# Kernel tuning notes

Hardware: AMD Instinct MI355X
Metric: run time of the kernel (lower is better)

Reference implementation:

```python
import jax, jax.numpy as jnp
import numpy as np

H, B, GH = 4096, 8192, 1024
TEMP = 1.0


def setup_inputs() -> dict:
    key = jax.random.key(0)
    ks = jax.random.split(key, 8)
    return {
        "hidden_states": jax.random.normal(ks[0], (B, H), jnp.float32),
        "attention_mask": jax.random.randint(ks[1], (B,), 0, 2) > 0,
        # similarity_proj: init N(0, 0.02); value_proj: nonzero randoms so kernel math is exercised
        "W_sim": jax.random.normal(ks[2], (H, H), jnp.float32) * 0.02,
        "W_val": jax.random.normal(ks[3], (H, H), jnp.float32) * 0.02,
        # gate_net: Linear(2H, GH) -> GELU -> Linear(GH, H) -> Sigmoid
        "W_g1": jax.random.normal(ks[4], (GH, 2 * H), jnp.float32) * 0.01,
        "b_g1": jnp.zeros((GH,), jnp.float32),
        "W_g2": jax.random.normal(ks[5], (H, GH), jnp.float32) * 0.01,
        "b_g2": jnp.full((H,), -3.0, jnp.float32),
    }


def reference(hidden_states, attention_mask, W_sim, W_val, W_g1, b_g1, W_g2, b_g2):
    b = hidden_states.shape[0]
    # similarity projection + L2 normalize (F.normalize, eps=1e-12)
    proj = hidden_states @ W_sim.T                                  # [B, H]
    norm = jnp.maximum(jnp.linalg.norm(proj, axis=-1, keepdims=True), 1e-12)
    normed = proj / norm
    sim = (normed @ normed.T) / TEMP                                # [B, B]
    # mask self (eye) and invalid samples (columns)
    eye = jnp.eye(b, dtype=bool)
    sim = jnp.where(eye | ~attention_mask[None, :], -jnp.inf, sim)
    weights = jax.nn.softmax(sim, axis=-1)
    weights = jnp.nan_to_num(weights, nan=0.0)
    values = hidden_states @ W_val.T                                # [B, H]
    cross = weights @ values                                        # [B, H]
    # question-aware gate: sigmoid(MLP(cat(h, cross)))
    gate_in = jnp.concatenate([hidden_states, cross], axis=-1)      # [B, 2H]
    h1 = jax.nn.gelu(gate_in @ W_g1.T + b_g1, approximate=False)    # exact GELU (torch default)
    gate = jax.nn.sigmoid(h1 @ W_g2.T + b_g2)                       # [B, H]
    return hidden_states + gate * cross
```

## Files before the change

### kernel.cpp

```cpp
#include <hip/hip_runtime.h>


#define HDIM 4096
#define BATCH 8192
#define GHDIM 1024

typedef unsigned short u16;
typedef short bf16x8 __attribute__((ext_vector_type(8)));
typedef float f32x4 __attribute__((ext_vector_type(4)));

__device__ __forceinline__ u16 f2bf(float f) {
  union { float f; unsigned u; } v; v.f = f;
  unsigned r = v.u + 0x7FFFu + ((v.u >> 16) & 1u);
  return (u16)(r >> 16);
}
__device__ __forceinline__ float bf2f(u16 u) {
  union { unsigned u; float f; } v; v.u = ((unsigned)u) << 16;
  return v.f;
}

__global__ void cast_f32_bf16(const float* __restrict__ src, u16* __restrict__ dst, int n4) {
  int i = blockIdx.x * 256 + threadIdx.x;
  if (i < n4) {
    float4 f = ((const float4*)src)[i];
    ushort4 o;
    o.x = f2bf(f.x); o.y = f2bf(f.y); o.z = f2bf(f.z); o.w = f2bf(f.w);
    ((ushort4*)dst)[i] = o;
  }
}

__global__ void detect_mask(const unsigned char* __restrict__ m, int nbytes, int* __restrict__ flag) {
  __shared__ int cnt[256];
  int c = 0;
  for (int i = threadIdx.x; i < nbytes; i += 256)
    if ((i & 3) && m[i]) c++;
  cnt[threadIdx.x] = c;
  __syncthreads();
  for (int s = 128; s > 0; s >>= 1) {
    if ((int)threadIdx.x < s) cnt[threadIdx.x] += cnt[threadIdx.x + s];
    __syncthreads();
  }
  if (threadIdx.x == 0) *flag = cnt[0];
}

__global__ void compact_mask(const void* __restrict__ raw, const int* __restrict__ flag,
                             int* __restrict__ idxc, int* __restrict__ kinfo) {
  const int t = threadIdx.x;
  const bool isbool = (*flag > 0);
  __shared__ int cnt[256];
  __shared__ int total;
  const int base0 = t * 32;
  int c = 0;
  for (int i = 0; i < 32; i++) {
    int gi = base0 + i;
    int v = isbool ? ((const unsigned char*)raw)[gi] : ((const int*)raw)[gi];
    if (v) c++;
  }
  cnt[t] = c;
  __syncthreads();
  if (t == 0) {
    int acc = 0;
    for (int i = 0; i < 256; i++) { int x = cnt[i]; cnt[i] = acc; acc += x; }
    total = acc;
    kinfo[0] = acc;
    kinfo[1] = (acc + 255) & ~255;
  }
  __syncthreads();
  int w = cnt[t];
  for (int i = 0; i < 32; i++) {
    int gi = base0 + i;
    int v = isbool ? ((const unsigned char*)raw)[gi] : ((const int*)raw)[gi];
    if (v) idxc[w++] = gi;
  }
  for (int i = total + t; i < BATCH; i += 256) idxc[i] = -1;
}

__global__ void gather_rows(const u16* __restrict__ src, u16* __restrict__ dst,
                            const int* __restrict__ idxc, const int* __restrict__ kinfo) {
  int c = blockIdx.x;
  int kc = kinfo[0], kp = kinfo[1];
  if (c >= kp) return;
  uint4* d = (uint4*)(dst + (size_t)c * HDIM);
  if (c < kc) {
    const uint4* s = (const uint4*)(src + (size_t)idxc[c] * HDIM);
    d[threadIdx.x] = s[threadIdx.x];
    d[threadIdx.x + 256] = s[threadIdx.x + 256];
  } else {
    uint4 z = {0, 0, 0, 0};
    d[threadIdx.x] = z;
    d[threadIdx.x + 256] = z;
  }
}

__global__ void normalize_rows(u16* __restrict__ p) {
  int row = blockIdx.x;
  uint4* r = (uint4*)(p + (size_t)row * HDIM);
  uint4 d[2];
  float s = 0.f;
#pragma unroll
  for (int i = 0; i < 2; i++) {
    d[i] = r[i * 256 + threadIdx.x];
    const u16* u = (const u16*)&d[i];
#pragma unroll
    for (int j = 0; j < 8; j++) { float f = bf2f(u[j]); s += f * f; }
  }
  __shared__ float red[256];
  red[threadIdx.x] = s;
  __syncthreads();
  for (int st = 128; st > 0; st >>= 1) {
    if ((int)threadIdx.x < st) red[threadIdx.x] += red[threadIdx.x + st];
    __syncthreads();
  }
  float scale = 1.0f / fmaxf(sqrtf(red[0]), 1e-12f);
#pragma unroll
  for (int i = 0; i < 2; i++) {
    u16* u = (u16*)&d[i];
#pragma unroll
    for (int j = 0; j < 8; j++) u[j] = f2bf(bf2f(u[j]) * scale);
    r[i * 256 + threadIdx.x] = d[i];
  }
}

__global__ void softmax_rows_dyn(u16* __restrict__ sim, const int* __restrict__ kinfo) {
  const int kp = kinfo[1];
  const int row = blockIdx.x;
  uint4* r = (uint4*)(sim + (size_t)row * BATCH);
  float v[32];
  int active[4];
  float mx = -3.0e38f;
#pragma unroll
  for (int ch = 0; ch < 4; ch++) {
    int base = ch * 2048 + threadIdx.x * 8;
    active[ch] = (base < kp);
    if (active[ch]) {
      uint4 d = r[ch * 256 + threadIdx.x];
      const u16* u = (const u16*)&d;
#pragma unroll
      for (int j = 0; j < 8; j++) {
        float f = bf2f(u[j]);
        v[ch * 8 + j] = f;
        mx = fmaxf(mx, f);
      }
    }
  }
  __shared__ float red[256];
  red[threadIdx.x] = mx;
  __syncthreads();
  for (int st = 128; st > 0; st >>= 1) {
    if ((int)threadIdx.x < st) red[threadIdx.x] = fmaxf(red[threadIdx.x], red[threadIdx.x + st]);
    __syncthreads();
  }
  mx = red[0];
  __syncthreads();
  float s = 0.f;
#pragma unroll
  for (int ch = 0; ch < 4; ch++) {
    if (active[ch]) {
#pragma unroll
      for (int j = 0; j < 8; j++) {
        float e = (v[ch * 8 + j] < -1.0e30f) ? 0.f : __expf(v[ch * 8 + j] - mx);
        v[ch * 8 + j] = e;
        s += e;
      }
    }
  }
  red[threadIdx.x] = s;
  __syncthreads();
  for (int st = 128; st > 0; st >>= 1) {
    if ((int)threadIdx.x < st) red[threadIdx.x] += red[threadIdx.x + st];
    __syncthreads();
  }
  float inv = (red[0] > 0.f) ? 1.0f / red[0] : 0.f;
#pragma unroll
  for (int ch = 0; ch < 4; ch++) {
    if (active[ch]) {
      uint4 d;
      u16* u = (u16*)&d;
#pragma unroll
      for (int j = 0; j < 8; j++) u[j] = f2bf(v[ch * 8 + j] * inv);
      r[ch * 256 + threadIdx.x] = d;
    }
  }
}

enum { EPI_BF16 = 0, EPI_SIM = 1, EPI_F32 = 2, EPI_GELU = 3, EPI_FINAL = 4 };

__device__ __forceinline__ void async_load16(const u16* g, u16* l) {
  __builtin_amdgcn_global_load_lds(
      (const __attribute__((address_space(1))) void*)g,
      (__attribute__((address_space(3))) void*)l, 16, 0, 0);
}

template <int EPI>
__global__ __launch_bounds__(512, 2) void gemm256(
    const u16* __restrict__ A, int lda,
    const u16* __restrict__ B, int ldb,
    void* __restrict__ C, int ldc,
    int M, int N, int K,
    const int* __restrict__ kinfo, int dynN, int dynK,
    const int* __restrict__ idxc,
    const float* __restrict__ aux,
    const u16* __restrict__ aux2,
    const float* __restrict__ bias) {
  const int nwg = (int)(gridDim.x * gridDim.y);
  const int orig = (int)(blockIdx.y * gridDim.x + blockIdx.x);
  int wgid;
  {
    int q = nwg >> 3, r = nwg & 7, x = orig & 7, lo = orig >> 3;
    wgid = (x < r ? x * (q + 1) : r * (q + 1) + (x - r) * q) + lo;
  }
  const int bx = wgid % (int)gridDim.x;
  const int by = wgid / (int)gridDim.x;
  const int rowBase = by * 256;
  const int colBase = bx * 256;
  if (dynN && colBase >= kinfo[1]) return;
  const int Keff = dynK ? kinfo[1] : K;
  const int NT = Keff >> 5;

  __shared__ __align__(16) u16 sm[4 * 16384];

  const int tid = threadIdx.x;
  const int lane = tid & 63, wave = tid >> 6;
  const int wm = wave >> 2, wn = wave & 3;
  const int fr = lane & 15, kq = lane >> 4;

  int aOff[8], bOff[4];
#pragma unroll
  for (int mi = 0; mi < 8; mi++) {
    int lin = ((wm * 8 + mi) << 10) + (fr << 6) + (kq << 4);
    aOff[mi] = lin ^ (((fr >> 3) & 1) << 5);
  }
#pragma unroll
  for (int ni = 0; ni < 4; ni++) {
    int lin = ((wn * 4 + ni) << 10) + (fr << 6) + (kq << 4);
    bOff[ni] = (lin ^ (((fr >> 3) & 1) << 5)) + 16384;
  }

  const int i0row = wave * 16 + (lane >> 2);
  const int scol = ((lane & 3) << 3) ^ (((lane >> 5) & 1) << 4);

  auto stageA = [&](int tt) {
    const int sb = (tt & 3) * 16384;
    const int kt = tt << 5;
#pragma unroll
    for (int i = 0; i < 2; i++)
      async_load16(A + (size_t)(rowBase + i * 128 + i0row) * lda + kt + scol,
                   sm + sb + i * 4096 + tid * 8);
  };
  auto stageB = [&](int tt) {
    const int sb = (tt & 3) * 16384 + 8192;
    const int kt = tt << 5;
#pragma unroll
    for (int i = 0; i < 2; i++)
      async_load16(B + (size_t)(colBase + i * 128 + i0row) * ldb + kt + scol,
                   sm + sb + i * 4096 + tid * 8);
  };

  f32x4 zero = {0.f, 0.f, 0.f, 0.f};
  f32x4 acc[8][4];
#pragma unroll
  for (int mi = 0; mi < 8; mi++)
#pragma unroll
    for (int ni = 0; ni < 4; ni++) acc[mi][ni] = zero;

  if (NT > 0) { stageA(0); stageB(0); }
  if (NT > 1) { stageA(1); stageB(1); }
  if (NT > 2) { stageA(2); stageB(2); }
  if (NT >= 3)      asm volatile("s_waitcnt vmcnt(8)" ::: "memory");
  else if (NT == 2) asm volatile("s_waitcnt vmcnt(4)" ::: "memory");
  else              asm volatile("s_waitcnt vmcnt(0)" ::: "memory");
  __builtin_amdgcn_sched_barrier(0);
  __builtin_amdgcn_s_barrier();

  for (int t = 0; t < NT; ++t) {
    const char* slot = (const char*)sm + (size_t)(t & 3) * 32768;
    const int pt = t + 3;
    const bool pf = pt < NT;

    bf16x8 af[4], bf[4];
#pragma unroll
    for (int mi = 0; mi < 4; mi++) af[mi] = *(const bf16x8*)(slot + aOff[mi]);
#pragma unroll
    for (int ni = 0; ni < 4; ni++) bf[ni] = *(const bf16x8*)(slot + bOff[ni]);
    if (pf) stageA(pt);
    __builtin_amdgcn_s_barrier();
    __builtin_amdgcn_s_setprio(1);
#pragma unroll
    for (int mi = 0; mi < 4; mi++)
#pragma unroll
      for (int ni = 0; ni < 4; ni++)
        acc[mi][ni] = __builtin_amdgcn_mfma_f32_16x16x32_bf16(af[mi], bf[ni], acc[mi][ni], 0, 0, 0);
    __builtin_amdgcn_s_setprio(0);
    __builtin_amdgcn_s_barrier();

#pragma unroll
    for (int mi = 0; mi < 4; mi++) af[mi] = *(const bf16x8*)(slot + aOff[mi + 4]);
    if (pf) stageB(pt);
    __builtin_amdgcn_s_barrier();
    __builtin_amdgcn_s_setprio(1);
#pragma unroll
    for (int mi = 0; mi < 4; mi++)
#pragma unroll
      for (int ni = 0; ni < 4; ni++)
        acc[mi + 4][ni] = __builtin_amdgcn_mfma_f32_16x16x32_bf16(af[mi], bf[ni], acc[mi + 4][ni], 0, 0, 0);
    __builtin_amdgcn_s_setprio(0);
    if (pf)                asm volatile("s_waitcnt vmcnt(8)" ::: "memory");
    else if (t + 2 < NT)   asm volatile("s_waitcnt vmcnt(4)" ::: "memory");
    else if (t + 1 < NT)   asm volatile("s_waitcnt vmcnt(0)" ::: "memory");
    __builtin_amdgcn_sched_barrier(0);
    __builtin_amdgcn_s_barrier();
  }

  const int quad = lane >> 4, lcol = lane & 15;
#pragma unroll
  for (int mi = 0; mi < 8; mi++) {
#pragma unroll
    for (int ni = 0; ni < 4; ni++) {
#pragma unroll
      for (int r = 0; r < 4; r++) {
        int grow = rowBase + wm * 128 + mi * 16 + quad * 4 + r;
        int gcol = colBase + wn * 64 + ni * 16 + lcol;
        float v = acc[mi][ni][r];
        size_t idx = (size_t)grow * ldc + gcol;
        if constexpr (EPI == EPI_BF16) {
          ((u16*)C)[idx] = f2bf(v);
        } else if constexpr (EPI == EPI_SIM) {
          bool dead = (gcol >= kinfo[0]) || (idxc[gcol] == grow);
          ((u16*)C)[idx] = dead ? (u16)0xFF80 : f2bf(v);
        } else if constexpr (EPI == EPI_F32) {
          ((float*)C)[idx] = v;
        } else if constexpr (EPI == EPI_GELU) {
          float x = v + aux[idx] + bias[gcol];
          float g = 0.5f * x * (1.0f + erff(x * 0.70710678118654752f));
          ((u16*)C)[idx] = f2bf(g);
        } else {
          float x = v + bias[gcol];
          float g = 1.0f / (1.0f + __expf(-x));
          ((float*)C)[idx] = aux[idx] + g * bf2f(aux2[idx]);
        }
      }
    }
  }
}

template <int EPI>
__global__ __launch_bounds__(256) void gemm_bt(
    const u16* __restrict__ A, int lda,
    const u16* __restrict__ B, int ldb,
    void* __restrict__ C, int ldc,
    int M, int N, int K,
    const int* __restrict__ kinfo, int dynN, int dynK,
    const int* __restrict__ idxc,
    const float* __restrict__ aux,
    const u16* __restrict__ aux2,
    const float* __restrict__ bias) {
  const int rowBase = blockIdx.y * 128;
  const int colBase = blockIdx.x * 128;
  if (dynN && colBase >= kinfo[1]) return;
  const int Keff = dynK ? kinfo[1] : K;

  __shared__ __align__(16) u16 lA[128 * 64];
  __shared__ __align__(16) u16 lB[128 * 64];
  const int tid = threadIdx.x;
  const int lane = tid & 63;
  const int wave = tid >> 6;
  const int waveRow = (wave >> 1) * 64;
  const int waveCol = (wave & 1) * 64;

  const u16* Ab = A + (size_t)rowBase * lda;
  const u16* Bb = B + (size_t)colBase * ldb;

  f32x4 zero = {0.f, 0.f, 0.f, 0.f};
  f32x4 acc[4][4];
#pragma unroll
  for (int mi = 0; mi < 4; mi++)
#pragma unroll
    for (int ni = 0; ni < 4; ni++) acc[mi][ni] = zero;

  for (int kt = 0; kt < Keff; kt += 64) {
#pragma unroll
    for (int i = 0; i < 4; i++) {
      int c = i * 256 + tid;
      int row = c >> 3, k8 = c & 7;
      int gk8 = k8 ^ (row & 7);
      async_load16(Ab + (size_t)row * lda + kt + gk8 * 8, &lA[c * 8]);
    }
#pragma unroll
    for (int i = 0; i < 4; i++) {
      int c = i * 256 + tid;
      int row = c >> 3, k8 = c & 7;
      int gk8 = k8 ^ (row & 7);
      async_load16(Bb + (size_t)row * ldb + kt + gk8 * 8, &lB[c * 8]);
    }
    __syncthreads();
#pragma unroll
    for (int ks = 0; ks < 2; ks++) {
      const int kq = ks * 4 + (lane >> 4);
      bf16x8 af[4], bfr[4];
#pragma unroll
      for (int mi = 0; mi < 4; mi++) {
        int row = waveRow + mi * 16 + (lane & 15);
        af[mi] = *(const bf16x8*)&lA[row * 64 + ((kq ^ (row & 7)) * 8)];
      }
#pragma unroll
      for (int ni = 0; ni < 4; ni++) {
        int row = waveCol + ni * 16 + (lane & 15);
        bfr[ni] = *(const bf16x8*)&lB[row * 64 + ((kq ^ (row & 7)) * 8)];
      }
#pragma unroll
      for (int mi = 0; mi < 4; mi++)
#pragma unroll
        for (int ni = 0; ni < 4; ni++)
          acc[mi][ni] = __builtin_amdgcn_mfma_f32_16x16x32_bf16(af[mi], bfr[ni], acc[mi][ni], 0, 0, 0);
    }
    __syncthreads();
  }

  const int quad = lane >> 4, lcol = lane & 15;
#pragma unroll
  for (int mi = 0; mi < 4; mi++) {
#pragma unroll
    for (int ni = 0; ni < 4; ni++) {
#pragma unroll
      for (int r = 0; r < 4; r++) {
        int grow = rowBase + waveRow + mi * 16 + quad * 4 + r;
        int gcol = colBase + waveCol + ni * 16 + lcol;
        float v = acc[mi][ni][r];
        size_t idx = (size_t)grow * ldc + gcol;
        if constexpr (EPI == EPI_BF16) {
          ((u16*)C)[idx] = f2bf(v);
        } else if constexpr (EPI == EPI_SIM) {
          bool dead = (gcol >= kinfo[0]) || (idxc[gcol] == grow);
          ((u16*)C)[idx] = dead ? (u16)0xFF80 : f2bf(v);
        } else if constexpr (EPI == EPI_F32) {
          ((float*)C)[idx] = v;
        } else if constexpr (EPI == EPI_GELU) {
          float x = v + aux[idx] + bias[gcol];
          float g = 0.5f * x * (1.0f + erff(x * 0.70710678118654752f));
          ((u16*)C)[idx] = f2bf(g);
        } else {
          float x = v + bias[gcol];
          float g = 1.0f / (1.0f + __expf(-x));
          ((float*)C)[idx] = aux[idx] + g * bf2f(aux2[idx]);
        }
      }
    }
  }
}

extern "C" void kernel_launch(void* const* d_in, const int* in_sizes, int n_in,
                              void* d_out, int out_size, void* d_ws, size_t ws_size,
                              hipStream_t stream) {
  const float* hs   = (const float*)d_in[0];
  const void*  mraw = d_in[1];
  const float* Wsim = (const float*)d_in[2];
  const float* Wval = (const float*)d_in[3];
  const float* Wg1  = (const float*)d_in[4];
  const float* bg1  = (const float*)d_in[5];
  const float* Wg2  = (const float*)d_in[6];
  const float* bg2  = (const float*)d_in[7];
  float* out = (float*)d_out;

  char* ws = (char*)d_ws;
  size_t off = 0;
  auto alloc = [&](size_t bytes) {
    char* p = ws + off;
    off += (bytes + 255) & ~(size_t)255;
    return p;
  };
  u16* hidden_bf = (u16*)alloc((size_t)BATCH * HDIM * 2);
  u16* wbuf      = (u16*)alloc((size_t)HDIM * HDIM * 2);
  u16* r1        = (u16*)alloc((size_t)BATCH * HDIM * 2);
  u16* r2        = (u16*)alloc((size_t)BATCH * HDIM * 2);
  int* idxc      = (int*)alloc((size_t)BATCH * 4);
  int* kinfo     = (int*)alloc(256);
  int* flag      = (int*)alloc(256);
  if (off > ws_size) return;

  u16*   simw  = (u16*)d_out;
  float* h1acc = (float*)d_out;
  (void)in_sizes; (void)n_in; (void)out_size;

  dim3 blk(256);
  dim3 blk5(512);

  detect_mask<<<1, 256, 0, stream>>>((const unsigned char*)mraw, BATCH, flag);
  compact_mask<<<1, 256, 0, stream>>>(mraw, flag, idxc, kinfo);

  cast_f32_bf16<<<(BATCH * HDIM / 4) / 256, 256, 0, stream>>>(hs, hidden_bf, BATCH * HDIM / 4);

  cast_f32_bf16<<<(HDIM * HDIM / 4) / 256, 256, 0, stream>>>(Wsim, wbuf, HDIM * HDIM / 4);
  gemm256<EPI_BF16><<<dim3(HDIM / 256, BATCH / 256), blk5, 0, stream>>>(
      hidden_bf, HDIM, wbuf, HDIM, r1, HDIM, BATCH, HDIM, HDIM,
      nullptr, 0, 0, nullptr, nullptr, nullptr, nullptr);
  normalize_rows<<<BATCH, 256, 0, stream>>>(r1);

  gather_rows<<<BATCH, 256, 0, stream>>>(r1, r2, idxc, kinfo);

  gemm256<EPI_SIM><<<dim3(BATCH / 256, BATCH / 256), blk5, 0, stream>>>(
      r1, HDIM, r2, HDIM, simw, BATCH, BATCH, BATCH, HDIM,
      kinfo, 1, 0, idxc, nullptr, nullptr, nullptr);
  softmax_rows_dyn<<<BATCH, 256, 0, stream>>>(simw, kinfo);

  gather_rows<<<BATCH, 256, 0, stream>>>(hidden_bf, r1, idxc, kinfo);

  cast_f32_bf16<<<(HDIM * HDIM / 4) / 256, 256, 0, stream>>>(Wval, wbuf, HDIM * HDIM / 4);
  gemm256<EPI_BF16><<<dim3(BATCH / 256, HDIM / 256), blk5, 0, stream>>>(
      wbuf, HDIM, r1, HDIM, r2, BATCH, HDIM, BATCH, HDIM,
      kinfo, 1, 0, nullptr, nullptr, nullptr, nullptr);

  gemm256<EPI_BF16><<<dim3(HDIM / 256, BATCH / 256), blk5, 0, stream>>>(
      simw, BATCH, r2, BATCH, r1, HDIM, BATCH, HDIM, BATCH,
      kinfo, 0, 1, nullptr, nullptr, nullptr, nullptr);

  cast_f32_bf16<<<(GHDIM * 2 * HDIM / 4) / 256, 256, 0, stream>>>(Wg1, wbuf, GHDIM * 2 * HDIM / 4);
  gemm_bt<EPI_F32><<<dim3(GHDIM / 128, BATCH / 128), blk, 0, stream>>>(
      hidden_bf, HDIM, wbuf, 2 * HDIM, h1acc, GHDIM, BATCH, GHDIM, HDIM,
      nullptr, 0, 0, nullptr, nullptr, nullptr, nullptr);
  gemm_bt<EPI_GELU><<<dim3(GHDIM / 128, BATCH / 128), blk, 0, stream>>>(
      r1, HDIM, wbuf + HDIM, 2 * HDIM, r2, GHDIM, BATCH, GHDIM, HDIM,
      nullptr, 0, 0, nullptr, h1acc, nullptr, bg1);

  cast_f32_bf16<<<(HDIM * GHDIM / 4) / 256, 256, 0, stream>>>(Wg2, wbuf, HDIM * GHDIM / 4);
  gemm256<EPI_FINAL><<<dim3(HDIM / 256, BATCH / 256), blk5, 0, stream>>>(
      r2, GHDIM, wbuf, GHDIM, out, HDIM, BATCH, HDIM, GHDIM,
      nullptr, 0, 0, nullptr, hs, r1, bg2);
}
```

Baseline: 1.842 ms.

## Software-pipeline LDS fragment loads with double-buffered registers in GEMM main loop

Restructures the GEMM main loop to process two K-tiles per iteration with double-buffered register fragments (a0/a1, b0/b1). LDS reads for the next MFMA quad are issued before the current quad's MFMAs, with explicit lgkmcnt waits, so shared-memory latency overlaps with matrix math. The change also reduces barriers per tile and reorders the global prefetch waits. It raises register pressure and assumes NT is even, since the loop steps by two.

```diff
diff --git a/kernel.cpp b/kernel.cpp
--- a/kernel.cpp
+++ b/kernel.cpp
@@ -266,50 +266,82 @@
   if (NT > 0) { stageA(0); stageB(0); }
   if (NT > 1) { stageA(1); stageB(1); }
   if (NT > 2) { stageA(2); stageB(2); }
-  if (NT >= 3)      asm volatile("s_waitcnt vmcnt(8)" ::: "memory");
-  else if (NT == 2) asm volatile("s_waitcnt vmcnt(4)" ::: "memory");
-  else              asm volatile("s_waitcnt vmcnt(0)" ::: "memory");
+  if (NT > 2)      asm volatile("s_waitcnt vmcnt(8)" ::: "memory");
+  else if (NT > 1) asm volatile("s_waitcnt vmcnt(4)" ::: "memory");
+  else             asm volatile("s_waitcnt vmcnt(0)" ::: "memory");
   __builtin_amdgcn_sched_barrier(0);
   __builtin_amdgcn_s_barrier();
 
-  for (int t = 0; t < NT; ++t) {
-    const char* slot = (const char*)sm + (size_t)(t & 3) * 32768;
-    const int pt = t + 3;
-    const bool pf = pt < NT;
-
-    bf16x8 af[4], bf[4];
-#pragma unroll
-    for (int mi = 0; mi < 4; mi++) af[mi] = *(const bf16x8*)(slot + aOff[mi]);
-#pragma unroll
-    for (int ni = 0; ni < 4; ni++) bf[ni] = *(const bf16x8*)(slot + bOff[ni]);
-    if (pf) stageA(pt);
-    __builtin_amdgcn_s_barrier();
-    __builtin_amdgcn_s_setprio(1);
-#pragma unroll
-    for (int mi = 0; mi < 4; mi++)
-#pragma unroll
-      for (int ni = 0; ni < 4; ni++)
-        acc[mi][ni] = __builtin_amdgcn_mfma_f32_16x16x32_bf16(af[mi], bf[ni], acc[mi][ni], 0, 0, 0);
-    __builtin_amdgcn_s_setprio(0);
-    __builtin_amdgcn_s_barrier();
-
-#pragma unroll
-    for (int mi = 0; mi < 4; mi++) af[mi] = *(const bf16x8*)(slot + aOff[mi + 4]);
-    if (pf) stageB(pt);
-    __builtin_amdgcn_s_barrier();
-    __builtin_amdgcn_s_setprio(1);
-#pragma unroll
-    for (int mi = 0; mi < 4; mi++)
-#pragma unroll
-      for (int ni = 0; ni < 4; ni++)
-        acc[mi + 4][ni] = __builtin_amdgcn_mfma_f32_16x16x32_bf16(af[mi], bf[ni], acc[mi + 4][ni], 0, 0, 0);
-    __builtin_amdgcn_s_setprio(0);
-    if (pf)                asm volatile("s_waitcnt vmcnt(8)" ::: "memory");
-    else if (t + 2 < NT)   asm volatile("s_waitcnt vmcnt(4)" ::: "memory");
-    else if (t + 1 < NT)   asm volatile("s_waitcnt vmcnt(0)" ::: "memory");
+  bf16x8 a0[4], a1[4], b0[4], b1[4];
+  {
+    const char* s0 = (const char*)sm;
+#pragma unroll
+    for (int mi = 0; mi < 4; mi++) a0[mi] = *(const bf16x8*)(s0 + aOff[mi]);
+#pragma unroll
+    for (int ni = 0; ni < 4; ni++) b0[ni] = *(const bf16x8*)(s0 + bOff[ni]);
+  }
+
+#define MFMA_QUAD(AF, BF, OFS)                                                        \
+  __builtin_amdgcn_s_setprio(1);                                                      \
+  _Pragma("unroll") for (int mi = 0; mi < 4; mi++)                                    \
+      _Pragma("unroll") for (int ni = 0; ni < 4; ni++)                                \
+          acc[mi + OFS][ni] =                                                         \
+              __builtin_amdgcn_mfma_f32_16x16x32_bf16(AF[mi], BF[ni], acc[mi + OFS][ni], 0, 0, 0); \
+  __builtin_amdgcn_s_setprio(0);
+
+  for (int t = 0; t < NT; t += 2) {
+    const char* sT  = (const char*)sm + (size_t)((t    ) & 3) * 32768;
+    const char* sT1 = (const char*)sm + (size_t)((t + 1) & 3) * 32768;
+    const char* sT2 = (const char*)sm + (size_t)((t + 2) & 3) * 32768;
+
+#pragma unroll
+    for (int mi = 0; mi < 4; mi++) a1[mi] = *(const bf16x8*)(sT + aOff[mi + 4]);
+    if (t + 3 < NT) stageA(t + 3);
+    asm volatile("s_waitcnt lgkmcnt(4)" ::: "memory");
+    __builtin_amdgcn_sched_barrier(0);
+    MFMA_QUAD(a0, b0, 0)
+    if (t + 3 < NT)      asm volatile("s_waitcnt vmcnt(6)" ::: "memory");
+    else if (t + 2 < NT) asm volatile("s_waitcnt vmcnt(4)" ::: "memory");
+    else if (t + 1 < NT) asm volatile("s_waitcnt vmcnt(0)" ::: "memory");
     __builtin_amdgcn_sched_barrier(0);
     __builtin_amdgcn_s_barrier();
-  }
+
+#pragma unroll
+    for (int mi = 0; mi < 4; mi++) a0[mi] = *(const bf16x8*)(sT1 + aOff[mi]);
+#pragma unroll
+    for (int ni = 0; ni < 4; ni++) b1[ni] = *(const bf16x8*)(sT1 + bOff[ni]);
+    if (t + 3 < NT) stageB(t + 3);
+    asm volatile("s_waitcnt lgkmcnt(8)" ::: "memory");
+    __builtin_amdgcn_sched_barrier(0);
+    MFMA_QUAD(a1, b0, 4)
+    __builtin_amdgcn_s_barrier();
+
+#pragma unroll
+    for (int mi = 0; mi < 4; mi++) a1[mi] = *(const bf16x8*)(sT1 + aOff[mi + 4]);
+    if (t + 4 < NT) stageA(t + 4);
+    asm volatile("s_waitcnt lgkmcnt(4)" ::: "memory");
+    __builtin_amdgcn_sched_barrier(0);
+    MFMA_QUAD(a0, b1, 0)
+    if (t + 4 < NT)      asm volatile("s_waitcnt vmcnt(6)" ::: "memory");
+    else if (t + 3 < NT) asm volatile("s_waitcnt vmcnt(4)" ::: "memory");
+    else if (t + 2 < NT) asm volatile("s_waitcnt vmcnt(0)" ::: "memory");
+    __builtin_amdgcn_sched_barrier(0);
+    __builtin_amdgcn_s_barrier();
+
+    if (t + 2 < NT) {
+#pragma unroll
+      for (int mi = 0; mi < 4; mi++) a0[mi] = *(const bf16x8*)(sT2 + aOff[mi]);
+#pragma unroll
+      for (int ni = 0; ni < 4; ni++) b0[ni] = *(const bf16x8*)(sT2 + bOff[ni]);
+    }
+    if (t + 4 < NT) stageB(t + 4);
+    if (t + 2 < NT) asm volatile("s_waitcnt lgkmcnt(8)" ::: "memory");
+    else            asm volatile("s_waitcnt lgkmcnt(0)" ::: "memory");
+    __builtin_amdgcn_sched_barrier(0);
+    MFMA_QUAD(a1, b1, 4)
+    __builtin_amdgcn_s_barrier();
+  }
+#undef MFMA_QUAD
 
   const int quad = lane >> 4, lcol = lane & 15;
 #pragma unroll
```

After: 1.808 ms. Within noise of the previous version (-1.9%).

## Restructure 256x256 GEMM into quadrant-ordered K64 pipeline with 5-slot ring

Applied to the files above, without the earlier changes.

Rewrites the main loop of the 256x256 bf16 GEMM kernel. Each K step is now 64 wide instead of 32, and every wave computes four 64x32 quadrants using fragments loaded with an XOR-swizzled 128-byte row layout. Half-tiles are staged asynchronously into a five-slot LDS ring, and the A and B halves are interleaved between the quadrant MFMA phases with lgkmcnt and vmcnt waits. The intent is to hide global loads and LDS reads behind MFMA and to cut the number of barriers per unit of K. In exchange it uses more LDS, which may lower occupancy, and K must now be a multiple of 64.

```diff
diff --git a/kernel.cpp b/kernel.cpp
--- a/kernel.cpp
+++ b/kernel.cpp
@@ -215,128 +215,166 @@
   const int colBase = bx * 256;
   if (dynN && colBase >= kinfo[1]) return;
   const int Keff = dynK ? kinfo[1] : K;
-  const int NT = Keff >> 5;
-
-  __shared__ __align__(16) u16 sm[4 * 16384];
+  const int NT = Keff >> 6;
+
+  __shared__ __align__(16) u16 sm[81920];
 
   const int tid = threadIdx.x;
   const int lane = tid & 63, wave = tid >> 6;
   const int wm = wave >> 2, wn = wave & 3;
   const int fr = lane & 15, kq = lane >> 4;
 
-  int aOff[8], bOff[4];
-#pragma unroll
-  for (int mi = 0; mi < 8; mi++) {
-    int lin = ((wm * 8 + mi) << 10) + (fr << 6) + (kq << 4);
-    aOff[mi] = lin ^ (((fr >> 3) & 1) << 5);
-  }
-#pragma unroll
-  for (int ni = 0; ni < 4; ni++) {
-    int lin = ((wn * 4 + ni) << 10) + (fr << 6) + (kq << 4);
-    bOff[ni] = (lin ^ (((fr >> 3) & 1) << 5)) + 16384;
-  }
-
-  const int i0row = wave * 16 + (lane >> 2);
-  const int scol = ((lane & 3) << 3) ^ (((lane >> 5) & 1) << 4);
-
-  auto stageA = [&](int tt) {
-    const int sb = (tt & 3) * 16384;
-    const int kt = tt << 5;
-#pragma unroll
-    for (int i = 0; i < 2; i++)
-      async_load16(A + (size_t)(rowBase + i * 128 + i0row) * lda + kt + scol,
-                   sm + sb + i * 4096 + tid * 8);
+  int aO[4][2], bO[2][2];
+#pragma unroll
+  for (int mi = 0; mi < 4; mi++)
+#pragma unroll
+    for (int ks = 0; ks < 2; ks++) {
+      int R = wm * 64 + mi * 16 + fr;
+      int c16 = kq + ks * 4;
+      aO[mi][ks] = (R << 7) + ((c16 ^ (R & 7)) << 4);
+    }
+#pragma unroll
+  for (int ni = 0; ni < 2; ni++)
+#pragma unroll
+    for (int ks = 0; ks < 2; ks++) {
+      int R = wn * 32 + ni * 16 + fr;
+      int c16 = kq + ks * 4;
+      bO[ni][ks] = (R << 7) + ((c16 ^ (R & 7)) << 4);
+    }
+
+  const int rT = tid >> 3;
+  const int cT = ((tid ^ (tid >> 3)) & 7) * 8;
+  const u16* Abs = A + (size_t)(rowBase + rT) * lda + cT;
+  const u16* Bbs = B + (size_t)(colBase + rT) * ldb + cT;
+
+  auto stA = [&](int t, int h, int s) {
+    const u16* src = Abs + (size_t)(h * 128) * lda + t * 64;
+    u16* dst = sm + s * 8192 + tid * 8;
+    async_load16(src, dst);
+    async_load16(src + (size_t)64 * lda, dst + 4096);
   };
-  auto stageB = [&](int tt) {
-    const int sb = (tt & 3) * 16384 + 8192;
-    const int kt = tt << 5;
-#pragma unroll
-    for (int i = 0; i < 2; i++)
-      async_load16(B + (size_t)(colBase + i * 128 + i0row) * ldb + kt + scol,
-                   sm + sb + i * 4096 + tid * 8);
+  auto stB = [&](int t, int h, int s) {
+    const u16* src = Bbs + (size_t)(h * 128) * ldb + t * 64;
+    u16* dst = sm + 40960 + s * 8192 + tid * 8;
+    async_load16(src, dst);
+    async_load16(src + (size_t)64 * ldb, dst + 4096);
   };
 
   f32x4 zero = {0.f, 0.f, 0.f, 0.f};
-  f32x4 acc[8][4];
-#pragma unroll
-  for (int mi = 0; mi < 8; mi++)
-#pragma unroll
-    for (int ni = 0; ni < 4; ni++) acc[mi][ni] = zero;
-
-  if (NT > 0) { stageA(0); stageB(0); }
-  if (NT > 1) { stageA(1); stageB(1); }
-  if (NT > 2) { stageA(2); stageB(2); }
-  if (NT >= 3)      asm volatile("s_waitcnt vmcnt(8)" ::: "memory");
-  else if (NT == 2) asm volatile("s_waitcnt vmcnt(4)" ::: "memory");
-  else              asm volatile("s_waitcnt vmcnt(0)" ::: "memory");
-  __builtin_amdgcn_sched_barrier(0);
+  f32x4 acc[4][4][2];
+#pragma unroll
+  for (int q = 0; q < 4; q++)
+#pragma unroll
+    for (int mi = 0; mi < 4; mi++)
+#pragma unroll
+      for (int ni = 0; ni < 2; ni++) acc[q][mi][ni] = zero;
+
+  stA(0, 0, 0); stB(0, 0, 0); stA(0, 1, 1); stB(0, 1, 1);
+  if (NT > 1) {
+    stA(1, 0, 2); stB(1, 0, 2); stA(1, 1, 3);
+    asm volatile("s_waitcnt vmcnt(6)" ::: "memory");
+  } else {
+    asm volatile("s_waitcnt vmcnt(0)" ::: "memory");
+  }
   __builtin_amdgcn_s_barrier();
 
-  for (int t = 0; t < NT; ++t) {
-    const char* slot = (const char*)sm + (size_t)(t & 3) * 32768;
-    const int pt = t + 3;
-    const bool pf = pt < NT;
-
-    bf16x8 af[4], bf[4];
-#pragma unroll
-    for (int mi = 0; mi < 4; mi++) af[mi] = *(const bf16x8*)(slot + aOff[mi]);
-#pragma unroll
-    for (int ni = 0; ni < 4; ni++) bf[ni] = *(const bf16x8*)(slot + bOff[ni]);
-    if (pf) stageA(pt);
-    __builtin_amdgcn_s_barrier();
-    __builtin_amdgcn_s_setprio(1);
+  bf16x8 aF[4][2], b0F[2][2], b1F[2][2];
+
+#define MQUAD(Q, AF, BF)                                                       \
+  __builtin_amdgcn_s_setprio(1);                                               \
+  _Pragma("unroll") for (int mi = 0; mi < 4; mi++)                             \
+  _Pragma("unroll") for (int ni = 0; ni < 2; ni++)                             \
+  _Pragma("unroll") for (int ks = 0; ks < 2; ks++)                             \
+      acc[Q][mi][ni] = __builtin_amdgcn_mfma_f32_16x16x32_bf16(                \
+          AF[mi][ks], BF[ni][ks], acc[Q][mi][ni], 0, 0, 0);                    \
+  __builtin_amdgcn_s_setprio(0);
+
+  int s0 = 0, s1 = 1;
+  for (int g = 0; g < NT; ++g) {
+    const char* smb = (const char*)sm;
+    const int aB0 = s0 * 16384, aB1 = s1 * 16384;
+    const int bB0 = 81920 + s0 * 16384, bB1 = 81920 + s1 * 16384;
+    int sB1n = s1 + 2; if (sB1n >= 5) sB1n -= 5;
+    int sX2 = s0 + 4;  if (sX2 >= 5) sX2 -= 5;
+    const int sA1n = s0;
+    const bool st1 = (g + 1 < NT), st2 = (g + 2 < NT);
+
 #pragma unroll
     for (int mi = 0; mi < 4; mi++)
 #pragma unroll
-      for (int ni = 0; ni < 4; ni++)
-        acc[mi][ni] = __builtin_amdgcn_mfma_f32_16x16x32_bf16(af[mi], bf[ni], acc[mi][ni], 0, 0, 0);
-    __builtin_amdgcn_s_setprio(0);
-    __builtin_amdgcn_s_barrier();
-
-#pragma unroll
-    for (int mi = 0; mi < 4; mi++) af[mi] = *(const bf16x8*)(slot + aOff[mi + 4]);
-    if (pf) stageB(pt);
-    __builtin_amdgcn_s_barrier();
-    __builtin_amdgcn_s_setprio(1);
+      for (int ks = 0; ks < 2; ks++) aF[mi][ks] = *(const bf16x8*)(smb + aB0 + aO[mi][ks]);
+#pragma unroll
+    for (int ni = 0; ni < 2; ni++)
+#pragma unroll
+      for (int ks = 0; ks < 2; ks++) b0F[ni][ks] = *(const bf16x8*)(smb + bB0 + bO[ni][ks]);
+    if (st1) stB(g + 1, 1, sB1n);
+    asm volatile("s_waitcnt lgkmcnt(8)");
+    __builtin_amdgcn_s_barrier();
+    asm volatile("s_waitcnt lgkmcnt(0)");
+    MQUAD(0, aF, b0F)
+    __builtin_amdgcn_s_barrier();
+
+#pragma unroll
+    for (int ni = 0; ni < 2; ni++)
+#pragma unroll
+      for (int ks = 0; ks < 2; ks++) b1F[ni][ks] = *(const bf16x8*)(smb + bB1 + bO[ni][ks]);
+    if (st2) stA(g + 2, 0, sX2);
+    __builtin_amdgcn_s_barrier();
+    asm volatile("s_waitcnt lgkmcnt(0)");
+    MQUAD(1, aF, b1F)
+    __builtin_amdgcn_s_barrier();
+
 #pragma unroll
     for (int mi = 0; mi < 4; mi++)
 #pragma unroll
-      for (int ni = 0; ni < 4; ni++)
-        acc[mi + 4][ni] = __builtin_amdgcn_mfma_f32_16x16x32_bf16(af[mi], bf[ni], acc[mi + 4][ni], 0, 0, 0);
-    __builtin_amdgcn_s_setprio(0);
-    if (pf)                asm volatile("s_waitcnt vmcnt(8)" ::: "memory");
-    else if (t + 2 < NT)   asm volatile("s_waitcnt vmcnt(4)" ::: "memory");
-    else if (t + 1 < NT)   asm volatile("s_waitcnt vmcnt(0)" ::: "memory");
-    __builtin_amdgcn_sched_barrier(0);
-    __builtin_amdgcn_s_barrier();
-  }
+      for (int ks = 0; ks < 2; ks++) aF[mi][ks] = *(const bf16x8*)(smb + aB1 + aO[mi][ks]);
+    if (st2) stB(g + 2, 0, sX2);
+    __builtin_amdgcn_s_barrier();
+    asm volatile("s_waitcnt lgkmcnt(0)");
+    MQUAD(2, aF, b0F)
+    __builtin_amdgcn_s_barrier();
+
+    if (st2) stA(g + 2, 1, sA1n);
+    __builtin_amdgcn_s_barrier();
+    MQUAD(3, aF, b1F)
+    if (st2) asm volatile("s_waitcnt vmcnt(6)" ::: "memory");
+    else     asm volatile("s_waitcnt vmcnt(0)" ::: "memory");
+    __builtin_amdgcn_s_barrier();
+
+    s0 += 2; if (s0 >= 5) s0 -= 5;
+    s1 += 2; if (s1 >= 5) s1 -= 5;
+  }
+#undef MQUAD
 
   const int quad = lane >> 4, lcol = lane & 15;
 #pragma unroll
-  for (int mi = 0; mi < 8; mi++) {
-#pragma unroll
-    for (int ni = 0; ni < 4; ni++) {
-#pragma unroll
-      for (int r = 0; r < 4; r++) {
-        int grow = rowBase + wm * 128 + mi * 16 + quad * 4 + r;
-        int gcol = colBase + wn * 64 + ni * 16 + lcol;
-        float v = acc[mi][ni][r];
-        size_t idx = (size_t)grow * ldc + gcol;
-        if constexpr (EPI == EPI_BF16) {
-          ((u16*)C)[idx] = f2bf(v);
-        } else if constexpr (EPI == EPI_SIM) {
-          bool dead = (gcol >= kinfo[0]) || (idxc[gcol] == grow);
-          ((u16*)C)[idx] = dead ? (u16)0xFF80 : f2bf(v);
-        } else if constexpr (EPI == EPI_F32) {
-          ((float*)C)[idx] = v;
-        } else if constexpr (EPI == EPI_GELU) {
-          float x = v + aux[idx] + bias[gcol];
-          float g = 0.5f * x * (1.0f + erff(x * 0.70710678118654752f));
-          ((u16*)C)[idx] = f2bf(g);
-        } else {
-          float x = v + bias[gcol];
-          float g = 1.0f / (1.0f + __expf(-x));
-          ((float*)C)[idx] = aux[idx] + g * bf2f(aux2[idx]);
+  for (int q = 0; q < 4; q++) {
+#pragma unroll
+    for (int mi = 0; mi < 4; mi++) {
+#pragma unroll
+      for (int ni = 0; ni < 2; ni++) {
+#pragma unroll
+        for (int r = 0; r < 4; r++) {
+          int grow = rowBase + (q >> 1) * 128 + wm * 64 + mi * 16 + quad * 4 + r;
+          int gcol = colBase + (q & 1) * 128 + wn * 32 + ni * 16 + lcol;
+          float v = acc[q][mi][ni][r];
+          size_t idx = (size_t)grow * ldc + gcol;
+          if constexpr (EPI == EPI_BF16) {
+            ((u16*)C)[idx] = f2bf(v);
+          } else if constexpr (EPI == EPI_SIM) {
+            bool dead = (gcol >= kinfo[0]) || (idxc[gcol] == grow);
+            ((u16*)C)[idx] = dead ? (u16)0xFF80 : f2bf(v);
+          } else if constexpr (EPI == EPI_F32) {
+            ((float*)C)[idx] = v;
+          } else if constexpr (EPI == EPI_GELU) {
+            float x = v + aux[idx] + bias[gcol];
+            float g = 0.5f * x * (1.0f + erff(x * 0.70710678118654752f));
+            ((u16*)C)[idx] = f2bf(g);
+          } else {
+            float x = v + bias[gcol];
+            float g = 1.0f / (1.0f + __expf(-x));
+            ((float*)C)[idx] = aux[idx] + g * bf2f(aux2[idx]);
+          }
         }
       }
     }
```

Result: faster. 1.800 ms (-2.3%).
